# Kernel optimization log

Measured on AMD Instinct MI355X. Metric: run time of the kernel, lower is better.

Reference implementation:

```python
import jax, jax.numpy as jnp
import numpy as np

WORD_TOTAL = 1_000_000
POS_TOTAL = 123
DIM = 50        # word embedding dim
DWPE = 5        # position embedding dim
C = 230         # conv filters (dimensionC)
WIN = 3         # conv window
REL = 53        # relationTotal
B = 1024        # bag size (number of sentences)
L = 128         # sentence length


def setup_inputs() -> dict:
    key = jax.random.key(0)
    ks = jax.random.split(key, 12)
    con = np.sqrt(6.0 / (C + REL))
    con1 = np.sqrt(6.0 / ((DWPE + DIM) * WIN))
    inp = {
        "sen": jax.random.randint(ks[0], (B, L), 0, WORD_TOTAL),
        "p1": jax.random.randint(ks[1], (B, L), 0, POS_TOTAL),
        "p2": jax.random.randint(ks[2], (B, L), 0, POS_TOTAL),
        "wordVec": jax.random.normal(ks[3], (WORD_TOTAL, DIM), jnp.float32) * 0.05,
        "posVec1": jax.random.normal(ks[4], (POS_TOTAL, DWPE), jnp.float32) * con1,
        "posVec2": jax.random.normal(ks[5], (POS_TOTAL, DWPE), jnp.float32) * con1,
        "Wv": jax.random.normal(ks[6], (WIN, DIM, C), jnp.float32) * 0.05,
        "Wp1": jax.random.normal(ks[7], (WIN, DWPE, C), jnp.float32) * 0.05,
        "Wp2": jax.random.normal(ks[8], (WIN, DWPE, C), jnp.float32) * 0.05,
        "bv": jnp.zeros((C,), jnp.float32),
        "bp1": jnp.zeros((C,), jnp.float32),
        "bp2": jnp.zeros((C,), jnp.float32),
        "attW": jax.random.normal(ks[9], (C, C), jnp.float32) * con,
        "MR": jax.random.normal(ks[10], (C, REL), jnp.float32) * 0.05,
        "MRb": jnp.zeros((REL,), jnp.float32),
        "rel": 7,
    }
    return inp


def _conv_full_width(emb, W):
    Lout = emb.shape[1] - WIN + 1
    wins = jnp.stack([emb[:, j:j + Lout, :] for j in range(WIN)], axis=0)
    return jnp.einsum('jbld,jdc->blc', wins, W)  # [B, Lout, C]


def reference(sen, p1, p2, wordVec, posVec1, posVec2, Wv, bv, Wp1, bp1, Wp2, bp2, attW, MR, MRb, rel):
    # ---- encode: per-sentence PCNN-style encoder, batched over the bag ----
    ev = wordVec[sen]   # [B, L, DIM]
    e1 = posVec1[p1]    # [B, L, DWPE]
    e2 = posVec2[p2]    # [B, L, DWPE]
    c = (_conv_full_width(ev, Wv) + bv
         + _conv_full_width(e1, Wp1) + bp1
         + _conv_full_width(e2, Wp2) + bp2)          # [B, Lout, C]
    cnn_output = jnp.tanh(jnp.max(c, axis=1))          # [B, C]
    # ---- selective attention over the bag (training=False: dropout identity) ----
    scores = (cnn_output @ attW) @ MR + MRb            # [B, REL]
    weight = jax.nn.softmax(scores[:, rel])            # [B] = exp/sum(exp)
    att_output = jnp.sum(weight[:, None] * cnn_output, axis=0)[None, :]  # [1, C]
    output = jax.nn.softmax(att_output @ MR + MRb)     # [1, REL]
    return (output, att_output, cnn_output, weight[:, None])
```

## Files before the change

### kernel.cpp

```cpp
#include <hip/hip_runtime.h>
#include <math.h>

#define CCH 230
#define REL 53
#define BAG 1024
#define SLEN 128
#define LOUT 126

typedef __bf16 bf16x8 __attribute__((ext_vector_type(8)));
typedef float f32x4 __attribute__((ext_vector_type(4)));

#define WS_BF_USHORTS (16 * 6 * 64 * 8)
#define WS_BSUM 24576
#define WS_V    24832
#define WS_SCORES 25088

__device__ __forceinline__ unsigned short f2bf(float f) {
    unsigned u = __builtin_bit_cast(unsigned, f);
    unsigned r = (u + 0x7fffu + ((u >> 16) & 1u)) >> 16;
    return (unsigned short)r;
}

__global__ void pa_kernel(const float* __restrict__ Wv, const float* __restrict__ Wp1,
                          const float* __restrict__ Wp2, const float* __restrict__ bv,
                          const float* __restrict__ bp1, const float* __restrict__ bp2,
                          const float* __restrict__ attW, const float* __restrict__ MR,
                          const int* __restrict__ relp, float* __restrict__ ws) {
    if (blockIdx.x < 193) {
        int idx = blockIdx.x * 256 + threadIdx.x;
        if (idx < WS_BF_USHORTS) {
            int j = idx & 7;
            int lane = (idx >> 3) & 63;
            int q = idx >> 9;
            int ks = q % 6, ntile = q / 6;
            int n = ntile * 16 + (lane & 15);
            int k = ks * 32 + (lane >> 4) * 8 + j;
            float v = 0.f;
            if (k < 180 && n < CCH) {
                int jw = k / 60;
                int d = k - jw * 60;
                if (d < 50)      v = Wv[(jw * 50 + d) * CCH + n];
                else if (d < 55) v = Wp1[(jw * 5 + (d - 50)) * CCH + n];
                else             v = Wp2[(jw * 5 + (d - 55)) * CCH + n];
            }
            ((unsigned short*)ws)[idx] = f2bf(v);
        } else {
            int ch = idx - WS_BF_USHORTS;
            float v = 0.f;
            if (ch < CCH) v = bv[ch] + bp1[ch] + bp2[ch];
            ws[WS_BSUM + ch] = v;
        }
    } else {
        int i = (blockIdx.x - 193) * 4 + (threadIdx.x >> 6);
        int lane = threadIdx.x & 63;
        if (i < CCH) {
            int rel = *relp;
            float s = 0.f;
            for (int j = lane; j < CCH; j += 64) s += attW[i * CCH + j] * MR[j * REL + rel];
            for (int off = 32; off > 0; off >>= 1) s += __shfl_down(s, off, 64);
            if (lane == 0) ws[WS_V + i] = s;
        }
    }
}

__global__ __launch_bounds__(256, 2) void conv_kernel(
    const int* __restrict__ sen, const int* __restrict__ p1, const int* __restrict__ p2,
    const float* __restrict__ wordVec, const float* __restrict__ posVec1,
    const float* __restrict__ posVec2, const float* __restrict__ ws,
    const float* __restrict__ MRb, const int* __restrict__ relp,
    float* __restrict__ cnn_out, float* __restrict__ scores) {
    __shared__ __align__(16) unsigned short x_lds[132 * 60];
    __shared__ int s_idx[3][SLEN];
    __shared__ float s_red[4];
    const int b = blockIdx.x;
    const int tid = threadIdx.x;

    if (tid < SLEN) {
        s_idx[0][tid] = sen[b * SLEN + tid];
        s_idx[1][tid] = p1[b * SLEN + tid];
        s_idx[2][tid] = p2[b * SLEN + tid];
    }
    __syncthreads();

    for (int slot = tid; slot < 132 * 4; slot += 256) {
        int l = slot >> 2, t = slot & 3;
        if (t < 3) {
            float v[16];
            if (l < SLEN) {
                const float* base = wordVec + s_idx[0][l] * 50 + t * 16;
                #pragma unroll
                for (int k2 = 0; k2 < 8; ++k2) {
                    float2 f = *reinterpret_cast<const float2*>(base + 2 * k2);
                    v[2 * k2] = f.x; v[2 * k2 + 1] = f.y;
                }
            } else {
                #pragma unroll
                for (int q = 0; q < 16; ++q) v[q] = 0.f;
            }
            ushort4 o[4];
            #pragma unroll
            for (int q = 0; q < 4; ++q) {
                o[q].x = f2bf(v[4 * q + 0]); o[q].y = f2bf(v[4 * q + 1]);
                o[q].z = f2bf(v[4 * q + 2]); o[q].w = f2bf(v[4 * q + 3]);
            }
            ushort4* dst = reinterpret_cast<ushort4*>(x_lds + l * 60 + t * 16);
            #pragma unroll
            for (int q = 0; q < 4; ++q) dst[q] = o[q];
        } else {
            float v[12];
            if (l < SLEN) {
                float2 wv = *reinterpret_cast<const float2*>(wordVec + s_idx[0][l] * 50 + 48);
                v[0] = wv.x; v[1] = wv.y;
                int i1 = s_idx[1][l] * 5, i2 = s_idx[2][l] * 5;
                #pragma unroll
                for (int j = 0; j < 5; ++j) { v[2 + j] = posVec1[i1 + j]; v[7 + j] = posVec2[i2 + j]; }
            } else {
                #pragma unroll
                for (int q = 0; q < 12; ++q) v[q] = 0.f;
            }
            ushort4 o[3];
            #pragma unroll
            for (int q = 0; q < 3; ++q) {
                o[q].x = f2bf(v[4 * q + 0]); o[q].y = f2bf(v[4 * q + 1]);
                o[q].z = f2bf(v[4 * q + 2]); o[q].w = f2bf(v[4 * q + 3]);
            }
            ushort4* dst = reinterpret_cast<ushort4*>(x_lds + l * 60 + 48);
            #pragma unroll
            for (int q = 0; q < 3; ++q) dst[q] = o[q];
        }
    }
    __syncthreads();

    const int lane = tid & 63, w = tid >> 6;
    const int quad = lane >> 4, l16 = lane & 15;
    const unsigned short* wsu = (const unsigned short*)ws;

    f32x4 acc[8][4];
    #pragma unroll
    for (int mt = 0; mt < 8; ++mt)
        #pragma unroll
        for (int nt = 0; nt < 4; ++nt) acc[mt][nt] = (f32x4){0.f, 0.f, 0.f, 0.f};

    union AU { uint2 u2[2]; bf16x8 v; };

    #pragma unroll
    for (int ks = 0; ks < 6; ++ks) {
        bf16x8 bfrag[4];
        #pragma unroll
        for (int nt = 0; nt < 4; ++nt) {
            int ntile = w * 4 + nt;
            bfrag[nt] = *reinterpret_cast<const bf16x8*>(wsu + ((ntile * 6 + ks) * 64 + lane) * 8);
        }
        int kg = ks * 4 + quad;
        #pragma unroll
        for (int mt = 0; mt < 8; ++mt) {
            int m = mt * 16 + l16;
            const uint2* ap = reinterpret_cast<const uint2*>(x_lds + m * 60 + kg * 8);
            AU a; a.u2[0] = ap[0]; a.u2[1] = ap[1];
            #pragma unroll
            for (int nt = 0; nt < 4; ++nt)
                acc[mt][nt] = __builtin_amdgcn_mfma_f32_16x16x32_bf16(a.v, bfrag[nt], acc[mt][nt], 0, 0, 0);
        }
    }

    float vals[4];
    #pragma unroll
    for (int nt = 0; nt < 4; ++nt) {
        float mv = -3.0e38f;
        #pragma unroll
        for (int mt = 0; mt < 8; ++mt) {
            #pragma unroll
            for (int r = 0; r < 4; ++r) {
                int l = mt * 16 + quad * 4 + r;
                if (l < LOUT) mv = fmaxf(mv, acc[mt][nt][r]);
            }
        }
        mv = fmaxf(mv, __shfl_xor(mv, 16, 64));
        mv = fmaxf(mv, __shfl_xor(mv, 32, 64));
        int ch = w * 64 + nt * 16 + l16;
        float t = tanhf(mv + ws[WS_BSUM + ch]);
        vals[nt] = t;
        if (quad == 0 && ch < CCH) cnn_out[b * CCH + ch] = t;
    }

    float s = 0.f;
    if (quad == 0) {
        #pragma unroll
        for (int nt = 0; nt < 4; ++nt) {
            int ch = w * 64 + nt * 16 + l16;
            if (ch < CCH) s += vals[nt] * ws[WS_V + ch];
        }
    }
    for (int off = 32; off > 0; off >>= 1) s += __shfl_down(s, off, 64);
    if (lane == 0) s_red[w] = s;
    __syncthreads();
    if (tid == 0) scores[b] = s_red[0] + s_red[1] + s_red[2] + s_red[3] + MRb[*relp];
}

__global__ void final_kernel(const float* __restrict__ cnn, const float* __restrict__ MR,
                             const float* __restrict__ MRb, const float* __restrict__ scores,
                             float* __restrict__ out0, float* __restrict__ att_out,
                             float* __restrict__ w_out) {
    __shared__ float red[1024];
    __shared__ float wbuf[1024];
    __shared__ float abuf[256];
    __shared__ float lbuf[64];
    __shared__ float MRs[CCH * REL];
    int tid = threadIdx.x;

    for (int i = tid; i < CCH * REL; i += 1024) MRs[i] = MR[i];

    float s = scores[tid];
    red[tid] = s; __syncthreads();
    for (int off = 512; off > 0; off >>= 1) {
        if (tid < off) red[tid] = fmaxf(red[tid], red[tid + off]);
        __syncthreads();
    }
    float mx = red[0]; __syncthreads();
    float e = expf(s - mx);
    red[tid] = e; __syncthreads();
    for (int off = 512; off > 0; off >>= 1) {
        if (tid < off) red[tid] += red[tid + off];
        __syncthreads();
    }
    float sum = red[0]; __syncthreads();
    float w = e / sum;
    w_out[tid] = w;
    wbuf[tid] = w;
    __syncthreads();

    int ch = tid & 255, grp = tid >> 8;
    float a = 0.f;
    if (ch < CCH) {
        int bb0 = grp * 256;
        #pragma unroll 16
        for (int bb = bb0; bb < bb0 + 256; ++bb) a += wbuf[bb] * cnn[bb * CCH + ch];
    }
    red[grp * 256 + ch] = a;
    __syncthreads();
    float t = 0.f;
    if (tid < 256) {
        float att = red[tid] + red[256 + tid] + red[512 + tid] + red[768 + tid];
        if (tid < CCH) { att_out[tid] = att; abuf[tid] = att; }
    }
    __syncthreads();
    if (tid < REL) {
        t = MRb[tid];
        #pragma unroll 10
        for (int c = 0; c < CCH; ++c) t += abuf[c] * MRs[c * REL + tid];
        lbuf[tid] = t;
    }
    __syncthreads();
    if (tid == 0) {
        float m2 = -3.0e38f;
        for (int i = 0; i < REL; ++i) m2 = fmaxf(m2, lbuf[i]);
        float s2 = 0.f;
        for (int i = 0; i < REL; ++i) s2 += expf(lbuf[i] - m2);
        lbuf[60] = m2; lbuf[61] = s2;
    }
    __syncthreads();
    if (tid < REL) out0[tid] = expf(t - lbuf[60]) / lbuf[61];
}

extern "C" void kernel_launch(void* const* d_in, const int* in_sizes, int n_in,
                              void* d_out, int out_size, void* d_ws, size_t ws_size,
                              hipStream_t stream) {
    const int* sen = (const int*)d_in[0];
    const int* p1  = (const int*)d_in[1];
    const int* p2  = (const int*)d_in[2];
    const float* wordVec = (const float*)d_in[3];
    const float* posVec1 = (const float*)d_in[4];
    const float* posVec2 = (const float*)d_in[5];
    const float* Wv  = (const float*)d_in[6];
    const float* Wp1 = (const float*)d_in[7];
    const float* Wp2 = (const float*)d_in[8];
    const float* bv  = (const float*)d_in[9];
    const float* bp1 = (const float*)d_in[10];
    const float* bp2 = (const float*)d_in[11];
    const float* attW = (const float*)d_in[12];
    const float* MR  = (const float*)d_in[13];
    const float* MRb = (const float*)d_in[14];
    const int* relp  = (const int*)d_in[15];

    float* ws = (float*)d_ws;
    float* out = (float*)d_out;
    float* out0    = out;
    float* att_out = out + REL;
    float* cnn_out = out + REL + CCH;
    float* w_out   = out + REL + CCH + BAG * CCH;

    hipLaunchKernelGGL(pa_kernel, dim3(193 + 58), dim3(256), 0, stream,
                       Wv, Wp1, Wp2, bv, bp1, bp2, attW, MR, relp, ws);
    hipLaunchKernelGGL(conv_kernel, dim3(BAG), dim3(256), 0, stream,
                       sen, p1, p2, wordVec, posVec1, posVec2, ws, MRb, relp,
                       cnn_out, ws + WS_SCORES);
    hipLaunchKernelGGL(final_kernel, dim3(1), dim3(1024), 0, stream,
                       cnn_out, MR, MRb, ws + WS_SCORES, out0, att_out, w_out);
}
```

Measured before the change: 317.5 us.

## Widen conv blocks to 512 threads with 2 N-tiles per wave and preloaded weights

```diff
diff --git a/kernel.cpp b/kernel.cpp
--- a/kernel.cpp
+++ b/kernel.cpp
@@ -63,7 +63,7 @@
     }
 }
 
-__global__ __launch_bounds__(256, 2) void conv_kernel(
+__global__ __launch_bounds__(512, 4) void conv_kernel(
     const int* __restrict__ sen, const int* __restrict__ p1, const int* __restrict__ p2,
     const float* __restrict__ wordVec, const float* __restrict__ posVec1,
     const float* __restrict__ posVec2, const float* __restrict__ ws,
@@ -71,86 +71,83 @@
     float* __restrict__ cnn_out, float* __restrict__ scores) {
     __shared__ __align__(16) unsigned short x_lds[132 * 60];
     __shared__ int s_idx[3][SLEN];
-    __shared__ float s_red[4];
+    __shared__ float s_red[8];
     const int b = blockIdx.x;
     const int tid = threadIdx.x;
-
-    if (tid < SLEN) {
-        s_idx[0][tid] = sen[b * SLEN + tid];
-        s_idx[1][tid] = p1[b * SLEN + tid];
-        s_idx[2][tid] = p2[b * SLEN + tid];
-    }
-    __syncthreads();
-
-    for (int slot = tid; slot < 132 * 4; slot += 256) {
-        int l = slot >> 2, t = slot & 3;
-        if (t < 3) {
-            float v[16];
-            if (l < SLEN) {
-                const float* base = wordVec + s_idx[0][l] * 50 + t * 16;
-                #pragma unroll
-                for (int k2 = 0; k2 < 8; ++k2) {
-                    float2 f = *reinterpret_cast<const float2*>(base + 2 * k2);
-                    v[2 * k2] = f.x; v[2 * k2 + 1] = f.y;
-                }
-            } else {
-                #pragma unroll
-                for (int q = 0; q < 16; ++q) v[q] = 0.f;
-            }
-            ushort4 o[4];
-            #pragma unroll
-            for (int q = 0; q < 4; ++q) {
-                o[q].x = f2bf(v[4 * q + 0]); o[q].y = f2bf(v[4 * q + 1]);
-                o[q].z = f2bf(v[4 * q + 2]); o[q].w = f2bf(v[4 * q + 3]);
-            }
-            ushort4* dst = reinterpret_cast<ushort4*>(x_lds + l * 60 + t * 16);
-            #pragma unroll
-            for (int q = 0; q < 4; ++q) dst[q] = o[q];
-        } else {
-            float v[12];
-            if (l < SLEN) {
-                float2 wv = *reinterpret_cast<const float2*>(wordVec + s_idx[0][l] * 50 + 48);
-                v[0] = wv.x; v[1] = wv.y;
-                int i1 = s_idx[1][l] * 5, i2 = s_idx[2][l] * 5;
-                #pragma unroll
-                for (int j = 0; j < 5; ++j) { v[2 + j] = posVec1[i1 + j]; v[7 + j] = posVec2[i2 + j]; }
-            } else {
-                #pragma unroll
-                for (int q = 0; q < 12; ++q) v[q] = 0.f;
-            }
-            ushort4 o[3];
-            #pragma unroll
-            for (int q = 0; q < 3; ++q) {
-                o[q].x = f2bf(v[4 * q + 0]); o[q].y = f2bf(v[4 * q + 1]);
-                o[q].z = f2bf(v[4 * q + 2]); o[q].w = f2bf(v[4 * q + 3]);
-            }
-            ushort4* dst = reinterpret_cast<ushort4*>(x_lds + l * 60 + 48);
-            #pragma unroll
-            for (int q = 0; q < 3; ++q) dst[q] = o[q];
-        }
-    }
-    __syncthreads();
-
     const int lane = tid & 63, w = tid >> 6;
     const int quad = lane >> 4, l16 = lane & 15;
     const unsigned short* wsu = (const unsigned short*)ws;
 
-    f32x4 acc[8][4];
+    bf16x8 bfrag[6][2];
+    #pragma unroll
+    for (int ks = 0; ks < 6; ++ks)
+        #pragma unroll
+        for (int nt = 0; nt < 2; ++nt) {
+            int ntile = w * 2 + nt;
+            bfrag[ks][nt] = *reinterpret_cast<const bf16x8*>(wsu + ((ntile * 6 + ks) * 64 + lane) * 8);
+        }
+
+    if (tid < 384) {
+        int a = tid >> 7, i = tid & 127;
+        const int* src = (a == 0) ? sen : (a == 1) ? p1 : p2;
+        s_idx[a][i] = src[b * SLEN + i];
+    }
+    __syncthreads();
+
+    {
+        int l = tid >> 2, t = tid & 3;
+        if (t < 3) {
+            float v[16];
+            const float* base = wordVec + s_idx[0][l] * 50 + t * 16;
+            #pragma unroll
+            for (int k2 = 0; k2 < 8; ++k2) {
+                float2 f = *reinterpret_cast<const float2*>(base + 2 * k2);
+                v[2 * k2] = f.x; v[2 * k2 + 1] = f.y;
+            }
+            ushort4* dst = reinterpret_cast<ushort4*>(x_lds + l * 60 + t * 16);
+            #pragma unroll
+            for (int q = 0; q < 4; ++q) {
+                ushort4 o;
+                o.x = f2bf(v[4 * q + 0]); o.y = f2bf(v[4 * q + 1]);
+                o.z = f2bf(v[4 * q + 2]); o.w = f2bf(v[4 * q + 3]);
+                dst[q] = o;
+            }
+        } else {
+            float v[12];
+            float2 wv = *reinterpret_cast<const float2*>(wordVec + s_idx[0][l] * 50 + 48);
+            v[0] = wv.x; v[1] = wv.y;
+            int i1 = s_idx[1][l] * 5, i2 = s_idx[2][l] * 5;
+            #pragma unroll
+            for (int j = 0; j < 5; ++j) { v[2 + j] = posVec1[i1 + j]; v[7 + j] = posVec2[i2 + j]; }
+            ushort4* dst = reinterpret_cast<ushort4*>(x_lds + l * 60 + 48);
+            #pragma unroll
+            for (int q = 0; q < 3; ++q) {
+                ushort4 o;
+                o.x = f2bf(v[4 * q + 0]); o.y = f2bf(v[4 * q + 1]);
+                o.z = f2bf(v[4 * q + 2]); o.w = f2bf(v[4 * q + 3]);
+                dst[q] = o;
+            }
+        }
+    }
+    if (tid < 16) {
+        int l = SLEN + (tid >> 2), t = tid & 3;
+        ushort4 z; z.x = z.y = z.z = z.w = 0;
+        ushort4* dst = reinterpret_cast<ushort4*>(x_lds + l * 60 + ((t < 3) ? t * 16 : 48));
+        if (t < 3) { dst[0] = z; dst[1] = z; dst[2] = z; dst[3] = z; }
+        else       { dst[0] = z; dst[1] = z; dst[2] = z; }
+    }
+    __syncthreads();
+
+    f32x4 acc[8][2];
     #pragma unroll
     for (int mt = 0; mt < 8; ++mt)
         #pragma unroll
-        for (int nt = 0; nt < 4; ++nt) acc[mt][nt] = (f32x4){0.f, 0.f, 0.f, 0.f};
+        for (int nt = 0; nt < 2; ++nt) acc[mt][nt] = (f32x4){0.f, 0.f, 0.f, 0.f};
 
     union AU { uint2 u2[2]; bf16x8 v; };
 
     #pragma unroll
     for (int ks = 0; ks < 6; ++ks) {
-        bf16x8 bfrag[4];
-        #pragma unroll
-        for (int nt = 0; nt < 4; ++nt) {
-            int ntile = w * 4 + nt;
-            bfrag[nt] = *reinterpret_cast<const bf16x8*>(wsu + ((ntile * 6 + ks) * 64 + lane) * 8);
-        }
         int kg = ks * 4 + quad;
         #pragma unroll
         for (int mt = 0; mt < 8; ++mt) {
@@ -158,14 +155,14 @@
             const uint2* ap = reinterpret_cast<const uint2*>(x_lds + m * 60 + kg * 8);
             AU a; a.u2[0] = ap[0]; a.u2[1] = ap[1];
             #pragma unroll
-            for (int nt = 0; nt < 4; ++nt)
-                acc[mt][nt] = __builtin_amdgcn_mfma_f32_16x16x32_bf16(a.v, bfrag[nt], acc[mt][nt], 0, 0, 0);
-        }
-    }
-
-    float vals[4];
+            for (int nt = 0; nt < 2; ++nt)
+                acc[mt][nt] = __builtin_amdgcn_mfma_f32_16x16x32_bf16(a.v, bfrag[ks][nt], acc[mt][nt], 0, 0, 0);
+        }
+    }
+
+    float vals[2];
     #pragma unroll
-    for (int nt = 0; nt < 4; ++nt) {
+    for (int nt = 0; nt < 2; ++nt) {
         float mv = -3.0e38f;
         #pragma unroll
         for (int mt = 0; mt < 8; ++mt) {
@@ -177,7 +174,7 @@
         }
         mv = fmaxf(mv, __shfl_xor(mv, 16, 64));
         mv = fmaxf(mv, __shfl_xor(mv, 32, 64));
-        int ch = w * 64 + nt * 16 + l16;
+        int ch = w * 32 + nt * 16 + l16;
         float t = tanhf(mv + ws[WS_BSUM + ch]);
         vals[nt] = t;
         if (quad == 0 && ch < CCH) cnn_out[b * CCH + ch] = t;
@@ -186,15 +183,20 @@
     float s = 0.f;
     if (quad == 0) {
         #pragma unroll
-        for (int nt = 0; nt < 4; ++nt) {
-            int ch = w * 64 + nt * 16 + l16;
+        for (int nt = 0; nt < 2; ++nt) {
+            int ch = w * 32 + nt * 16 + l16;
             if (ch < CCH) s += vals[nt] * ws[WS_V + ch];
         }
     }
     for (int off = 32; off > 0; off >>= 1) s += __shfl_down(s, off, 64);
     if (lane == 0) s_red[w] = s;
     __syncthreads();
-    if (tid == 0) scores[b] = s_red[0] + s_red[1] + s_red[2] + s_red[3] + MRb[*relp];
+    if (tid == 0) {
+        float t = MRb[*relp];
+        #pragma unroll
+        for (int i = 0; i < 8; ++i) t += s_red[i];
+        scores[b] = t;
+    }
 }
 
 __global__ void final_kernel(const float* __restrict__ cnn, const float* __restrict__ MR,
@@ -291,7 +293,7 @@
 
     hipLaunchKernelGGL(pa_kernel, dim3(193 + 58), dim3(256), 0, stream,
                        Wv, Wp1, Wp2, bv, bp1, bp2, attW, MR, relp, ws);
-    hipLaunchKernelGGL(conv_kernel, dim3(BAG), dim3(256), 0, stream,
+    hipLaunchKernelGGL(conv_kernel, dim3(BAG), dim3(512), 0, stream,
                        sen, p1, p2, wordVec, posVec1, posVec2, ws, MRb, relp,
                        cnn_out, ws + WS_SCORES);
     hipLaunchKernelGGL(final_kernel, dim3(1), dim3(1024), 0, stream,
```

Measured after the change: 314.5 us. About the same (-1.0%).
